# Kernel optimization log

Measured on AMD Instinct MI355X. Metric: run time of the kernel, lower is better.

## Reference

```python
import jax, jax.numpy as jnp
import numpy as np

N_HEADS, HEAD_D, N_LVL, N_PTS, EMB = 8, 32, 1, 4, 256


def _grid_sample(img, grid):
    """Bilinear grid_sample, align_corners=False, zeros padding.
    img: [N,C,H,W], grid: [N,Hg,Wg,2] in [-1,1] (x=width, y=height)."""
    N, C, H, W = img.shape
    x = (grid[..., 0] + 1.0) * (W * 0.5) - 0.5
    y = (grid[..., 1] + 1.0) * (H * 0.5) - 0.5
    x0 = jnp.floor(x); y0 = jnp.floor(y)
    x1 = x0 + 1.0; y1 = y0 + 1.0
    wx1 = x - x0; wx0 = 1.0 - wx1
    wy1 = y - y0; wy0 = 1.0 - wy1
    img_flat = img.reshape(N, C, H * W)

    def gather(xi, yi, w):
        xii = xi.astype(jnp.int32); yii = yi.astype(jnp.int32)
        valid = (xii >= 0) & (xii < W) & (yii >= 0) & (yii < H)
        lin = jnp.clip(yii, 0, H - 1) * W + jnp.clip(xii, 0, W - 1)   # [N,Hg,Wg]
        vals = jnp.take_along_axis(img_flat, lin.reshape(N, 1, -1), axis=2)
        vals = vals.reshape(N, C, lin.shape[1], lin.shape[2])
        return vals * (w * valid)[:, None]

    return (gather(x0, y0, wx0 * wy0) + gather(x1, y0, wx1 * wy0)
            + gather(x0, y1, wx0 * wy1) + gather(x1, y1, wx1 * wy1))


def setup_inputs() -> dict:
    key = jax.random.key(0)
    ks = jax.random.split(key, 16)
    bs, nq, Hl, Wl = 4, 10000, 100, 100
    nv = Hl * Wl
    s = 0.02
    return {
        "query": jax.random.normal(ks[0], (bs, nq, EMB), jnp.float32),
        "key": jax.random.normal(ks[1], (bs, nv, EMB), jnp.float32),
        "value": jax.random.normal(ks[2], (bs, nv, EMB), jnp.float32),
        "reference_points": jax.random.uniform(ks[3], (bs, nq, N_LVL, 2), jnp.float32),
        "Wq": s * jax.random.normal(ks[4], (HEAD_D, HEAD_D), jnp.float32),
        "bq": jnp.zeros((HEAD_D,), jnp.float32),
        "Wk": s * jax.random.normal(ks[5], (HEAD_D, HEAD_D), jnp.float32),
        "bk": jnp.zeros((HEAD_D,), jnp.float32),
        "Wv": s * jax.random.normal(ks[6], (HEAD_D, HEAD_D), jnp.float32),
        "bv": jnp.zeros((HEAD_D,), jnp.float32),
        "Woff": s * jax.random.normal(ks[7], (N_LVL * N_PTS * 2, HEAD_D), jnp.float32),
        "boff": jnp.zeros((N_LVL * N_PTS * 2,), jnp.float32),
        "Wo": s * jax.random.normal(ks[8], (EMB, EMB), jnp.float32),
        "bo": jnp.zeros((EMB,), jnp.float32),
        "spatial_shapes": jnp.array([[Hl, Wl]], dtype=jnp.int32),
    }


def reference(query, key, value, reference_points, Wq, bq, Wk, bk, Wv, bv,
              Woff, boff, Wo, bo, spatial_shapes):
    nH, D, nL, nP = N_HEADS, HEAD_D, N_LVL, N_PTS
    bs, nq, _ = query.shape
    ss = np.asarray(spatial_shapes)                      # static [L,2] (H,W)
    residual = query
    qh = query.reshape(bs, nq, nH, D)
    kh = key.reshape(bs, -1, nH, D)
    vh = value.reshape(bs, -1, nH, D)
    norm = jnp.asarray(np.stack([ss[:, 1], ss[:, 0]], -1), jnp.float32)  # (W,H) per level
    off = (qh @ Woff.T + boff).reshape(bs, nq, nH, nL, nP, 2)
    loc = reference_points[:, :, None, :, None, :] + off / norm[None, None, None, :, None, :]
    grids = 2.0 * loc - 1.0                              # [b,q,h,L,P,2]
    k_parts, v_parts = [], []
    start = 0
    for l in range(nL):
        Hl, Wl = int(ss[l, 0]), int(ss[l, 1])
        sl = slice(start, start + Hl * Wl); start += Hl * Wl
        k_img = kh[:, sl].reshape(bs, Hl * Wl, nH * D).transpose(0, 2, 1).reshape(bs * nH, D, Hl, Wl)
        v_img = vh[:, sl].reshape(bs, Hl * Wl, nH * D).transpose(0, 2, 1).reshape(bs * nH, D, Hl, Wl)
        # NOTE: key grid uses only the FIRST query's sampling locations (as in source: grids[:, :1])
        gk = grids[:, :1, :, l].transpose(0, 2, 1, 3, 4).reshape(bs * nH, 1, nP, 2)
        gv = grids[:, :, :, l].transpose(0, 2, 1, 3, 4).reshape(bs * nH, nq, nP, 2)
        k_parts.append(_grid_sample(k_img, gk))          # [bH, D, 1, P]
        v_parts.append(_grid_sample(v_img, gv))          # [bH, D, nq, P]
    k_samp = jnp.stack(k_parts, axis=-2).reshape(bs * nH, D, nL * nP)
    k_samp = k_samp.reshape(bs, nH, D, nL * nP).transpose(0, 3, 1, 2)     # [b, LP, h, d]
    v_samp = jnp.stack(v_parts, axis=-2).reshape(bs * nH, D, nq, nL * nP)  # [bH, d, q, LP]
    q = qh @ Wq.T + bq                                                    # [b, q, h, d]
    k = k_samp @ Wk.T + bk                                                # [b, LP, h, d]
    v = (v_samp.transpose(0, 2, 3, 1) @ Wv.T + bv).transpose(0, 3, 1, 2)  # [bH, d, q, LP]
    attn = jax.nn.softmax(jnp.einsum('bqhd,bkhd->bqhk', q, k), axis=-1)   # [b, q, h, LP]
    attn = attn.transpose(0, 2, 1, 3).reshape(bs * nH, 1, nq, nL * nP)
    out = (v * attn).sum(-1).reshape(bs, nH * D, nq).transpose(0, 2, 1)   # [b, q, E]
    return out @ Wo.T + bo + residual  # dropout is identity in eval mode
```

## Files before the change

### kernel.cpp

```cpp
#include <hip/hip_runtime.h>
#include <hip/hip_bf16.h>
#include <math.h>

#define NH   8
#define HD   32
#define NP   4
#define EMB  256
#define IMG_H 100
#define IMG_W 100
#define NQ   10000
#define NV   10000
#define BS   4

#define W4S 36
#define TS  2
#define TPL (IMG_W / TS)
#define TPB (TPL * TPL)

#define FENCE() asm volatile("" ::: "memory")

typedef __attribute__((ext_vector_type(8))) short bf16x8;
typedef __attribute__((ext_vector_type(4))) float f32x4;

#define KT_OFF    0
#define KB_OFF    16384
#define BO2_OFF   17408
#define WCF_OFF   18432
#define WCB_OFF   (18432 + 262144)
#define CNT_OFF   (WCB_OFF + 131072)
#define OFF_OFF   (CNT_OFF + 40000)
#define QIDX_OFF  (OFF_OFF + 40000)
#define PREB_OFF  ((QIDX_OFF + 160000 + 63) & ~63ULL)
#define WS_SORT   ((size_t)QIDX_OFF + 160000)
#define WS_FULL   ((size_t)PREB_OFF + (size_t)BS * NQ * EMB * 2)

__global__ __launch_bounds__(64) void k1_keys(
    const float* __restrict__ query, const float* __restrict__ key,
    const float* __restrict__ refp,  const float* __restrict__ Woff,
    const float* __restrict__ boff,  const float* __restrict__ Wk,
    const float* __restrict__ bk,    const float* __restrict__ Wq,
    const float* __restrict__ bq,
    float* __restrict__ kt, float* __restrict__ kb)
{
    int b = blockIdx.x >> 3, h = blockIdx.x & 7;
    __shared__ float q0[HD];
    __shared__ float off[8];
    __shared__ float ks[NP][HD];
    __shared__ float kkl[NP][HD];
    int l = threadIdx.x;

    if (l < HD) q0[l] = query[(size_t)(b * NQ) * EMB + h * HD + l];
    __syncthreads();

    if (l < 8) {
        float s = boff[l];
        #pragma unroll
        for (int d = 0; d < HD; ++d) s += q0[d] * Woff[l * HD + d];
        off[l] = s;
    }
    __syncthreads();

    if (l < HD) {
        float refx = refp[(size_t)(b * NQ) * 2 + 0];
        float refy = refp[(size_t)(b * NQ) * 2 + 1];
        for (int p = 0; p < NP; ++p) {
            float x = refx * IMG_W + off[p * 2 + 0] - 0.5f;
            float y = refy * IMG_H + off[p * 2 + 1] - 0.5f;
            float x0f = floorf(x), y0f = floorf(y);
            int ix0 = (int)x0f, iy0 = (int)y0f;
            float fx = x - x0f, fy = y - y0f;
            float acc = 0.f;
            #pragma unroll
            for (int cy = 0; cy < 2; ++cy)
                #pragma unroll
                for (int cx = 0; cx < 2; ++cx) {
                    int xi = ix0 + cx, yi = iy0 + cy;
                    if ((unsigned)xi < IMG_W && (unsigned)yi < IMG_H) {
                        float wgt = (cx ? fx : 1.f - fx) * (cy ? fy : 1.f - fy);
                        acc += wgt * key[((size_t)b * NV + yi * IMG_W + xi) * EMB + h * HD + l];
                    }
                }
            ks[p][l] = acc;
        }
    }
    __syncthreads();

    #pragma unroll
    for (int t = 0; t < 2; ++t) {
        int idx = l + 64 * t;
        int p = idx >> 5, dout = idx & 31;
        float s = bk[dout];
        #pragma unroll
        for (int d = 0; d < HD; ++d) s += Wk[dout * HD + d] * ks[p][d];
        kkl[p][dout] = s;
    }
    __syncthreads();

    #pragma unroll
    for (int t = 0; t < 2; ++t) {
        int idx = l + 64 * t;
        int p = idx >> 5, d = idx & 31;
        float s = 0.f;
        #pragma unroll
        for (int dd = 0; dd < HD; ++dd) s += Wq[dd * HD + d] * kkl[p][dd];
        kt[((b * NP + p) * NH + h) * HD + d] = s;
    }
    if (l < NP) {
        float s = 0.f;
        #pragma unroll
        for (int dd = 0; dd < HD; ++dd) s += bq[dd] * kkl[l][dd];
        kb[(b * NP + l) * NH + h] = s;
    }
}

__global__ __launch_bounds__(256) void kcomb(
    const float* __restrict__ Wo, const float* __restrict__ Wv,
    const float* __restrict__ bv, const float* __restrict__ bo,
    float* __restrict__ wcf, __hip_bfloat16* __restrict__ wcb,
    float* __restrict__ bo2)
{
    __shared__ float sWv[HD * HD];
    __shared__ float sWoR[EMB];
    __shared__ float sws[4];
    int e = blockIdx.x, col = threadIdx.x;
    *(float4*)&sWv[col * 4] = *(const float4*)(Wv + col * 4);
    sWoR[col] = Wo[(size_t)e * EMB + col];
    __syncthreads();

    int h = col >> 5, d = col & 31;
    float s = 0.f;
    #pragma unroll
    for (int dd = 0; dd < HD; ++dd) s += sWoR[h * HD + dd] * sWv[dd * HD + d];
    wcf[(size_t)e * EMB + col] = s;
    if (wcb) wcb[(size_t)e * EMB + col] = __float2bfloat16(s);

    float pb = bv[d] * sWoR[col];
    #pragma unroll
    for (int o = 1; o < 64; o <<= 1) pb += __shfl_xor(pb, o);
    if ((col & 63) == 0) sws[col >> 6] = pb;
    __syncthreads();
    if (col == 0) bo2[e] = bo[e] + sws[0] + sws[1] + sws[2] + sws[3];
}

__device__ __forceinline__ int tile_of(const float* refp, int gq) {
    float rx = refp[(size_t)gq * 2 + 0];
    float ry = refp[(size_t)gq * 2 + 1];
    int px = min(max((int)(rx * IMG_W), 0), IMG_W - 1);
    int py = min(max((int)(ry * IMG_H), 0), IMG_H - 1);
    return (py / TS) * TPL + (px / TS);
}

__global__ __launch_bounds__(256) void ksort_count(
    const float* __restrict__ refp, int* __restrict__ cnt)
{
    int gq = blockIdx.x * 256 + threadIdx.x;
    if (gq < BS * NQ) {
        int b = gq / NQ;
        atomicAdd(&cnt[b * TPB + tile_of(refp, gq)], 1);
    }
}

__global__ __launch_bounds__(64) void ksort_scan(
    const int* __restrict__ cnt, int* __restrict__ off)
{
    int b = blockIdx.x, lane = threadIdx.x;
    const int PER = (TPB + 63) / 64;
    int lsum[PER];
    int s = 0;
    #pragma unroll
    for (int i = 0; i < PER; ++i) {
        int t = lane * PER + i;
        int c = (t < TPB) ? cnt[b * TPB + t] : 0;
        lsum[i] = s; s += c;
    }
    int inc = s;
    #pragma unroll
    for (int o = 1; o < 64; o <<= 1) {
        int v = __shfl_up(inc, o);
        if (lane >= o) inc += v;
    }
    int excl = inc - s;
    #pragma unroll
    for (int i = 0; i < PER; ++i) {
        int t = lane * PER + i;
        if (t < TPB) off[b * TPB + t] = b * NQ + excl + lsum[i];
    }
}

__global__ __launch_bounds__(256) void ksort_scatter(
    const float* __restrict__ refp, int* __restrict__ off, int* __restrict__ qidx)
{
    int gq = blockIdx.x * 256 + threadIdx.x;
    if (gq < BS * NQ) {
        int b = gq / NQ;
        int slot = atomicAdd(&off[b * TPB + tile_of(refp, gq)], 1);
        qidx[slot] = gq;
    }
}

template<int BF16OUT>
__global__ __launch_bounds__(256) void k2s(
    const float* __restrict__ query, const float* __restrict__ value,
    const float* __restrict__ refp,
    const float* __restrict__ Woff, const float* __restrict__ boff,
    const float* __restrict__ kt, const float* __restrict__ kb,
    const int* __restrict__ qidx,
    float* __restrict__ pre, __hip_bfloat16* __restrict__ preb)
{
    __shared__ float sWoff[8 * W4S];
    __shared__ float sboff[8];
    __shared__ float skt[NP * NH * W4S];
    __shared__ float skb[NP * NH];
    __shared__ float qld[4][NH * W4S];
    __shared__ float offs[4][64];
    __shared__ float attnw[4][32];
    __shared__ int   soff4[4][32][4];
    __shared__ float swgt4[4][32][4];

    int tid = threadIdx.x;

    int bid = blockIdx.x;
    int wg = (bid & 7) * (BS * NQ / 4 / 8) + (bid >> 3);
    int b0 = (wg * 4) / NQ;

    for (int i = tid; i < 8 * HD; i += 256) sWoff[(i >> 5) * W4S + (i & 31)] = Woff[i];
    if (tid < 8)  sboff[tid] = boff[tid];
    {
        int j = tid * 4;
        *(float4*)&skt[(j >> 5) * W4S + (j & 31)] =
            *(const float4*)(kt + b0 * (NP * NH * HD) + j);
    }
    if (tid < NP * NH) skb[tid] = kb[b0 * (NP * NH) + tid];

    int w = tid >> 6, lane = tid & 63;
    int gq = qidx ? qidx[wg * 4 + w] : (wg * 4 + w);
    int b = b0;

    float4 qv = *(const float4*)(query + (size_t)gq * EMB + lane * 4);
    { int e = lane * 4; *(float4*)&qld[w][(e >> 5) * W4S + (e & 31)] = qv; }
    float refx = refp[(size_t)gq * 2 + 0];
    float refy = refp[(size_t)gq * 2 + 1];
    __syncthreads();

    int h = lane >> 3, t = lane & 7;

    float qr[HD];
    #pragma unroll
    for (int d = 0; d < HD; d += 4) {
        float4 v4 = *(const float4*)&qld[w][h * W4S + d];
        qr[d] = v4.x; qr[d + 1] = v4.y; qr[d + 2] = v4.z; qr[d + 3] = v4.w;
    }

    {
        float s = sboff[t];
        const float* wr = &sWoff[t * W4S];
        #pragma unroll
        for (int d = 0; d < HD; d += 4) {
            float4 ww = *(const float4*)(wr + d);
            s += qr[d]*ww.x + qr[d+1]*ww.y + qr[d+2]*ww.z + qr[d+3]*ww.w;
        }
        offs[w][h * 8 + t] = s;
    }

    float plog[NP];
    #pragma unroll
    for (int p = 0; p < NP; ++p) {
        const float* kr = &skt[(p * NH + h) * W4S];
        float s = 0.f;
        #pragma unroll
        for (int k = 0; k < 4; ++k) s += qr[t + 8 * k] * kr[t + 8 * k];
        plog[p] = s;
    }
    #pragma unroll
    for (int p = 0; p < NP; ++p) {
        plog[p] += __shfl_xor(plog[p], 1, 8);
        plog[p] += __shfl_xor(plog[p], 2, 8);
        plog[p] += __shfl_xor(plog[p], 4, 8);
        plog[p] += skb[p * NH + h];
    }
    {
        float mm = fmaxf(fmaxf(plog[0], plog[1]), fmaxf(plog[2], plog[3]));
        float e0 = __expf(plog[0]-mm), e1 = __expf(plog[1]-mm);
        float e2 = __expf(plog[2]-mm), e3 = __expf(plog[3]-mm);
        float inv = 1.f / (e0 + e1 + e2 + e3);
        if (t < 4) {
            float a = (t == 0) ? e0 : (t == 1) ? e1 : (t == 2) ? e2 : e3;
            attnw[w][h * 4 + t] = a * inv;
        }
    }
    FENCE();

    if (lane < 32) {
        int h2 = lane >> 2, p = lane & 3;
        float x = refx * IMG_W + offs[w][h2 * 8 + p * 2 + 0] - 0.5f;
        float y = refy * IMG_H + offs[w][h2 * 8 + p * 2 + 1] - 0.5f;
        float x0f = floorf(x), y0f = floorf(y);
        int ix0 = (int)x0f, iy0 = (int)y0f;
        float fx = x - x0f, fy = y - y0f;
        float aw = attnw[w][lane];
        float wx1 = fx * aw, wx0 = aw - wx1;
        int bbase = b * (NV * EMB) + h2 * HD;
        int   o4[4]; float g4[4];
        #pragma unroll
        for (int c = 0; c < 4; ++c) {
            int cx = c & 1, cy = c >> 1;
            int xi = ix0 + cx, yi = iy0 + cy;
            bool valid = ((unsigned)xi < IMG_W) & ((unsigned)yi < IMG_H);
            int xc = min(max(xi, 0), IMG_W - 1);
            int yc = min(max(yi, 0), IMG_H - 1);
            o4[c] = (bbase + (yc * IMG_W + xc) * EMB) * 4;
            float wv = (cx ? wx1 : wx0) * (cy ? fy : 1.f - fy);
            g4[c] = valid ? wv : 0.f;
        }
        int4   ov = {o4[0], o4[1], o4[2], o4[3]};
        float4 gv = {g4[0], g4[1], g4[2], g4[3]};
        *(int4*)&soff4[w][lane][0]   = ov;
        *(float4*)&swgt4[w][lane][0] = gv;
    }
    FENCE();

    {
        unsigned co = t * 16;
        const char* vb = (const char*)value;
        float4 acc = {0.f, 0.f, 0.f, 0.f};
        #pragma unroll
        for (int p = 0; p < NP; ++p) {
            int hp = h * 4 + p;
            int4   o4 = *(const int4*)&soff4[w][hp][0];
            float4 g4 = *(const float4*)&swgt4[w][hp][0];
            float4 v0 = *(const float4*)(vb + (unsigned)o4.x + co);
            float4 v1 = *(const float4*)(vb + (unsigned)o4.y + co);
            float4 v2 = *(const float4*)(vb + (unsigned)o4.z + co);
            float4 v3 = *(const float4*)(vb + (unsigned)o4.w + co);
            acc.x += g4.x*v0.x + g4.y*v1.x + g4.z*v2.x + g4.w*v3.x;
            acc.y += g4.x*v0.y + g4.y*v1.y + g4.z*v2.y + g4.w*v3.y;
            acc.z += g4.x*v0.z + g4.y*v1.z + g4.z*v2.z + g4.w*v3.z;
            acc.w += g4.x*v0.w + g4.y*v1.w + g4.z*v2.w + g4.w*v3.w;
        }
        int cb = t * 4;
        if (BF16OUT) {
            __hip_bfloat16 pk[4];
            pk[0] = __float2bfloat16(acc.x);
            pk[1] = __float2bfloat16(acc.y);
            pk[2] = __float2bfloat16(acc.z);
            pk[3] = __float2bfloat16(acc.w);
            *(ushort4*)((unsigned short*)preb + (size_t)gq * EMB + h * HD + cb) =
                *(const ushort4*)&pk[0];
        } else {
            *(float4*)(pre + (size_t)gq * EMB + h * HD + cb) = acc;
        }
    }
}

__global__ __launch_bounds__(256) void k3_mfma(
    const __hip_bfloat16* __restrict__ preb, const __hip_bfloat16* __restrict__ wcb,
    float* __restrict__ outp, const float* __restrict__ query,
    const float* __restrict__ bo2)
{
    int w = threadIdx.x >> 6, lane = threadIdx.x & 63;
    size_t m0 = (size_t)blockIdx.x * 64;
    int n0 = w * 64;
    int lr = lane & 15, lg = lane >> 4;

    const short* pa = (const short*)preb;
    const short* pb = (const short*)wcb;

    f32x4 acc[4][4];
    #pragma unroll
    for (int mt = 0; mt < 4; ++mt)
        #pragma unroll
        for (int nt = 0; nt < 4; ++nt) acc[mt][nt] = (f32x4){0.f, 0.f, 0.f, 0.f};

    #pragma unroll
    for (int k0 = 0; k0 < EMB; k0 += 32) {
        bf16x8 af[4], bf[4];
        #pragma unroll
        for (int mt = 0; mt < 4; ++mt)
            af[mt] = *(const bf16x8*)(pa + (m0 + mt * 16 + lr) * EMB + k0 + lg * 8);
        #pragma unroll
        for (int nt = 0; nt < 4; ++nt)
            bf[nt] = *(const bf16x8*)(pb + (size_t)(n0 + nt * 16 + lr) * EMB + k0 + lg * 8);
        #pragma unroll
        for (int mt = 0; mt < 4; ++mt)
            #pragma unroll
            for (int nt = 0; nt < 4; ++nt)
                acc[mt][nt] = __builtin_amdgcn_mfma_f32_16x16x32_bf16(
                    af[mt], bf[nt], acc[mt][nt], 0, 0, 0);
    }

    float bov[4];
    #pragma unroll
    for (int nt = 0; nt < 4; ++nt) bov[nt] = bo2[n0 + nt * 16 + lr];

    #pragma unroll
    for (int mt = 0; mt < 4; ++mt)
        #pragma unroll
        for (int q = 0; q < 4; ++q) {
            size_t row = m0 + mt * 16 + lg * 4 + q;
            const float* qrow = query + row * EMB;
            float* orow = outp + row * EMB;
            #pragma unroll
            for (int nt = 0; nt < 4; ++nt) {
                int col = n0 + nt * 16 + lr;
                orow[col] = acc[mt][nt][q] + bov[nt] + qrow[col];
            }
        }
}

__global__ __launch_bounds__(256) void k3_gemm(
    const float* __restrict__ pre, float* __restrict__ outp,
    const float* __restrict__ query, const float* __restrict__ wcf,
    const float* __restrict__ bo2)
{
    __shared__ float As[64 * EMB];
    int tid = threadIdx.x;
    size_t r0 = (size_t)blockIdx.x * 64;
    {
        const float4* src = (const float4*)(pre + r0 * EMB);
        float4* dst = (float4*)As;
        for (int i = tid; i < 64 * EMB / 4; i += 256) dst[i] = src[i];
    }
    __syncthreads();

    int w = tid >> 6, lane = tid & 63;
    int rb = w * 16;
    float acc[16][4];
    #pragma unroll
    for (int r = 0; r < 16; ++r)
        #pragma unroll
        for (int j = 0; j < 4; ++j) acc[r][j] = 0.f;

    for (int kc = 0; kc < EMB / 4; ++kc) {
        float4 wreg[4];
        #pragma unroll
        for (int j = 0; j < 4; ++j)
            wreg[j] = *(const float4*)&wcf[(size_t)(lane + 64 * j) * EMB + kc * 4];
        #pragma unroll
        for (int r = 0; r < 16; ++r) {
            float4 a = *(const float4*)&As[(rb + r) * EMB + kc * 4];
            #pragma unroll
            for (int j = 0; j < 4; ++j)
                acc[r][j] += a.x * wreg[j].x + a.y * wreg[j].y
                           + a.z * wreg[j].z + a.w * wreg[j].w;
        }
    }

    #pragma unroll
    for (int r = 0; r < 16; ++r) {
        size_t row = r0 + rb + r;
        #pragma unroll
        for (int j = 0; j < 4; ++j) {
            int c = lane + 64 * j;
            outp[row * EMB + c] = acc[r][j] + bo2[c] + query[row * EMB + c];
        }
    }
}

extern "C" void kernel_launch(void* const* d_in, const int* in_sizes, int n_in,
                              void* d_out, int out_size, void* d_ws, size_t ws_size,
                              hipStream_t stream) {
    const float* query = (const float*)d_in[0];
    const float* key   = (const float*)d_in[1];
    const float* value = (const float*)d_in[2];
    const float* refp  = (const float*)d_in[3];
    const float* Wq   = (const float*)d_in[4];
    const float* bq   = (const float*)d_in[5];
    const float* Wk   = (const float*)d_in[6];
    const float* bk   = (const float*)d_in[7];
    const float* Wv   = (const float*)d_in[8];
    const float* bv   = (const float*)d_in[9];
    const float* Woff = (const float*)d_in[10];
    const float* boff = (const float*)d_in[11];
    const float* Wo   = (const float*)d_in[12];
    const float* bo   = (const float*)d_in[13];
    (void)in_sizes; (void)n_in; (void)out_size;

    float* out = (float*)d_out;
    char*  ws  = (char*)d_ws;
    float* kt  = (float*)(ws + KT_OFF);
    float* kb  = (float*)(ws + KB_OFF);
    float* bo2 = (float*)(ws + BO2_OFF);
    float* wcf = (float*)(ws + WCF_OFF);
    __hip_bfloat16* wcb = (__hip_bfloat16*)(ws + WCB_OFF);

    bool have_sort = (ws_size >= WS_SORT);
    int* cnt  = (int*)(ws + CNT_OFF);
    int* off  = (int*)(ws + OFF_OFF);
    int* qidx = have_sort ? (int*)(ws + QIDX_OFF) : nullptr;

    if (have_sort) hipMemsetAsync(cnt, 0, BS * TPB * sizeof(int), stream);

    k1_keys<<<BS * NH, 64, 0, stream>>>(query, key, refp, Woff, boff, Wk, bk,
                                        Wq, bq, kt, kb);
    kcomb<<<EMB, 256, 0, stream>>>(Wo, Wv, bv, bo, wcf, wcb, bo2);

    if (have_sort) {
        int nthr = (BS * NQ + 255) / 256;
        ksort_count<<<nthr, 256, 0, stream>>>(refp, cnt);
        ksort_scan<<<BS, 64, 0, stream>>>(cnt, off);
        ksort_scatter<<<nthr, 256, 0, stream>>>(refp, off, qidx);
    }

    if (ws_size >= WS_FULL) {
        __hip_bfloat16* preb = (__hip_bfloat16*)(ws + PREB_OFF);
        k2s<1><<<BS * NQ / 4, 256, 0, stream>>>(query, value, refp, Woff, boff,
                                                kt, kb, qidx, nullptr, preb);
        k3_mfma<<<BS * NQ / 64, 256, 0, stream>>>(preb, wcb, out, query, bo2);
    } else {
        k2s<0><<<BS * NQ / 4, 256, 0, stream>>>(query, value, refp, Woff, boff,
                                                kt, kb, qidx, out, nullptr);
        k3_gemm<<<BS * NQ / 64, 256, 0, stream>>>(out, out, query, wcf, bo2);
    }
}
```

Measured before the change: 101.2 us.

## Process queries per spatial tile with an LDS-staged value window

Replaces the per-query sampling kernel with one block per 2x2 reference tile. Each block stages a 4x4 pixel window of the value tensor into LDS and loops over the queries sorted into that tile. Bilinear samples that fall inside the window read from LDS, and any wave with an out-of-window sample falls back to global loads. Separately, the key-prep and weight-combine kernels are merged into one launch to cut launch overhead. The risks are uneven per-tile query counts, a larger LDS footprint that lowers occupancy, and blocks that exit early on empty tiles.

```diff
diff --git a/kernel.cpp b/kernel.cpp
--- a/kernel.cpp
+++ b/kernel.cpp
@@ -16,6 +16,7 @@
 #define TS  2
 #define TPL (IMG_W / TS)
 #define TPB (TPL * TPL)
+#define HS  520
 
 #define FENCE() asm volatile("" ::: "memory")
 
@@ -31,115 +32,110 @@
 #define OFF_OFF   (CNT_OFF + 40000)
 #define QIDX_OFF  (OFF_OFF + 40000)
 #define PREB_OFF  ((QIDX_OFF + 160000 + 63) & ~63ULL)
-#define WS_SORT   ((size_t)QIDX_OFF + 160000)
 #define WS_FULL   ((size_t)PREB_OFF + (size_t)BS * NQ * EMB * 2)
 
-__global__ __launch_bounds__(64) void k1_keys(
+__global__ __launch_bounds__(256) void kprep(
     const float* __restrict__ query, const float* __restrict__ key,
     const float* __restrict__ refp,  const float* __restrict__ Woff,
     const float* __restrict__ boff,  const float* __restrict__ Wk,
     const float* __restrict__ bk,    const float* __restrict__ Wq,
     const float* __restrict__ bq,
-    float* __restrict__ kt, float* __restrict__ kb)
-{
-    int b = blockIdx.x >> 3, h = blockIdx.x & 7;
-    __shared__ float q0[HD];
-    __shared__ float off[8];
-    __shared__ float ks[NP][HD];
-    __shared__ float kkl[NP][HD];
-    int l = threadIdx.x;
-
-    if (l < HD) q0[l] = query[(size_t)(b * NQ) * EMB + h * HD + l];
-    __syncthreads();
-
-    if (l < 8) {
-        float s = boff[l];
-        #pragma unroll
-        for (int d = 0; d < HD; ++d) s += q0[d] * Woff[l * HD + d];
-        off[l] = s;
-    }
-    __syncthreads();
-
-    if (l < HD) {
-        float refx = refp[(size_t)(b * NQ) * 2 + 0];
-        float refy = refp[(size_t)(b * NQ) * 2 + 1];
-        for (int p = 0; p < NP; ++p) {
-            float x = refx * IMG_W + off[p * 2 + 0] - 0.5f;
-            float y = refy * IMG_H + off[p * 2 + 1] - 0.5f;
-            float x0f = floorf(x), y0f = floorf(y);
-            int ix0 = (int)x0f, iy0 = (int)y0f;
-            float fx = x - x0f, fy = y - y0f;
-            float acc = 0.f;
-            #pragma unroll
-            for (int cy = 0; cy < 2; ++cy)
-                #pragma unroll
-                for (int cx = 0; cx < 2; ++cx) {
-                    int xi = ix0 + cx, yi = iy0 + cy;
-                    if ((unsigned)xi < IMG_W && (unsigned)yi < IMG_H) {
-                        float wgt = (cx ? fx : 1.f - fx) * (cy ? fy : 1.f - fy);
-                        acc += wgt * key[((size_t)b * NV + yi * IMG_W + xi) * EMB + h * HD + l];
-                    }
-                }
-            ks[p][l] = acc;
-        }
-    }
-    __syncthreads();
-
-    #pragma unroll
-    for (int t = 0; t < 2; ++t) {
-        int idx = l + 64 * t;
-        int p = idx >> 5, dout = idx & 31;
-        float s = bk[dout];
-        #pragma unroll
-        for (int d = 0; d < HD; ++d) s += Wk[dout * HD + d] * ks[p][d];
-        kkl[p][dout] = s;
-    }
-    __syncthreads();
-
-    #pragma unroll
-    for (int t = 0; t < 2; ++t) {
-        int idx = l + 64 * t;
-        int p = idx >> 5, d = idx & 31;
-        float s = 0.f;
-        #pragma unroll
-        for (int dd = 0; dd < HD; ++dd) s += Wq[dd * HD + d] * kkl[p][dd];
-        kt[((b * NP + p) * NH + h) * HD + d] = s;
-    }
-    if (l < NP) {
-        float s = 0.f;
-        #pragma unroll
-        for (int dd = 0; dd < HD; ++dd) s += bq[dd] * kkl[l][dd];
-        kb[(b * NP + l) * NH + h] = s;
-    }
-}
-
-__global__ __launch_bounds__(256) void kcomb(
     const float* __restrict__ Wo, const float* __restrict__ Wv,
     const float* __restrict__ bv, const float* __restrict__ bo,
+    float* __restrict__ kt, float* __restrict__ kb,
     float* __restrict__ wcf, __hip_bfloat16* __restrict__ wcb,
     float* __restrict__ bo2)
 {
-    __shared__ float sWv[HD * HD];
-    __shared__ float sWoR[EMB];
-    __shared__ float sws[4];
-    int e = blockIdx.x, col = threadIdx.x;
-    *(float4*)&sWv[col * 4] = *(const float4*)(Wv + col * 4);
-    sWoR[col] = Wo[(size_t)e * EMB + col];
-    __syncthreads();
-
-    int h = col >> 5, d = col & 31;
-    float s = 0.f;
-    #pragma unroll
-    for (int dd = 0; dd < HD; ++dd) s += sWoR[h * HD + dd] * sWv[dd * HD + d];
-    wcf[(size_t)e * EMB + col] = s;
-    if (wcb) wcb[(size_t)e * EMB + col] = __float2bfloat16(s);
-
-    float pb = bv[d] * sWoR[col];
-    #pragma unroll
-    for (int o = 1; o < 64; o <<= 1) pb += __shfl_xor(pb, o);
-    if ((col & 63) == 0) sws[col >> 6] = pb;
-    __syncthreads();
-    if (col == 0) bo2[e] = bo[e] + sws[0] + sws[1] + sws[2] + sws[3];
+    if (blockIdx.x < EMB) {
+        __shared__ float sWv[HD * HD];
+        __shared__ float sWoR[EMB];
+        __shared__ float sws[4];
+        int e = blockIdx.x, col = threadIdx.x;
+        *(float4*)&sWv[col * 4] = *(const float4*)(Wv + col * 4);
+        sWoR[col] = Wo[(size_t)e * EMB + col];
+        __syncthreads();
+
+        int d = col & 31;
+        float s = 0.f;
+        #pragma unroll
+        for (int dd = 0; dd < HD; ++dd) s += sWoR[(col >> 5) * HD + dd] * sWv[dd * HD + d];
+        wcf[(size_t)e * EMB + col] = s;
+        if (wcb) wcb[(size_t)e * EMB + col] = __float2bfloat16(s);
+
+        float pb = bv[d] * sWoR[col];
+        #pragma unroll
+        for (int o = 1; o < 64; o <<= 1) pb += __shfl_xor(pb, o);
+        if ((col & 63) == 0) sws[col >> 6] = pb;
+        __syncthreads();
+        if (col == 0) bo2[e] = bo[e] + sws[0] + sws[1] + sws[2] + sws[3];
+    } else {
+        int bh = blockIdx.x - EMB;
+        int b = bh >> 3, h = bh & 7;
+        __shared__ float q0[HD];
+        __shared__ float off[8];
+        __shared__ float ks[NP][HD];
+        __shared__ float kkl[NP][HD];
+        int l = threadIdx.x;
+
+        if (l < HD) q0[l] = query[(size_t)(b * NQ) * EMB + h * HD + l];
+        __syncthreads();
+
+        if (l < 8) {
+            float s = boff[l];
+            #pragma unroll
+            for (int d = 0; d < HD; ++d) s += q0[d] * Woff[l * HD + d];
+            off[l] = s;
+        }
+        __syncthreads();
+
+        if (l < HD) {
+            float refx = refp[(size_t)(b * NQ) * 2 + 0];
+            float refy = refp[(size_t)(b * NQ) * 2 + 1];
+            for (int p = 0; p < NP; ++p) {
+                float x = refx * IMG_W + off[p * 2 + 0] - 0.5f;
+                float y = refy * IMG_H + off[p * 2 + 1] - 0.5f;
+                float x0f = floorf(x), y0f = floorf(y);
+                int ix0 = (int)x0f, iy0 = (int)y0f;
+                float fx = x - x0f, fy = y - y0f;
+                float acc = 0.f;
+                #pragma unroll
+                for (int cy = 0; cy < 2; ++cy)
+                    #pragma unroll
+                    for (int cx = 0; cx < 2; ++cx) {
+                        int xi = ix0 + cx, yi = iy0 + cy;
+                        if ((unsigned)xi < IMG_W && (unsigned)yi < IMG_H) {
+                            float wgt = (cx ? fx : 1.f - fx) * (cy ? fy : 1.f - fy);
+                            acc += wgt * key[((size_t)b * NV + yi * IMG_W + xi) * EMB + h * HD + l];
+                        }
+                    }
+                ks[p][l] = acc;
+            }
+        }
+        __syncthreads();
+
+        if (l < 128) {
+            int p = l >> 5, dout = l & 31;
+            float s = bk[dout];
+            #pragma unroll
+            for (int d = 0; d < HD; ++d) s += Wk[dout * HD + d] * ks[p][d];
+            kkl[p][dout] = s;
+        }
+        __syncthreads();
+
+        if (l < 128) {
+            int p = l >> 5, d = l & 31;
+            float s = 0.f;
+            #pragma unroll
+            for (int dd = 0; dd < HD; ++dd) s += Wq[dd * HD + d] * kkl[p][dd];
+            kt[((b * NP + p) * NH + h) * HD + d] = s;
+        }
+        if (l < NP) {
+            float s = 0.f;
+            #pragma unroll
+            for (int dd = 0; dd < HD; ++dd) s += bq[dd] * kkl[l][dd];
+            kb[(b * NP + l) * NH + h] = s;
+        }
+    }
 }
 
 __device__ __forceinline__ int tile_of(const float* refp, int gq) {
@@ -161,7 +157,7 @@
 }
 
 __global__ __launch_bounds__(64) void ksort_scan(
-    const int* __restrict__ cnt, int* __restrict__ off)
+    const int* __restrict__ cnt, int* __restrict__ offarr)
 {
     int b = blockIdx.x, lane = threadIdx.x;
     const int PER = (TPB + 63) / 64;
@@ -183,29 +179,228 @@
     #pragma unroll
     for (int i = 0; i < PER; ++i) {
         int t = lane * PER + i;
-        if (t < TPB) off[b * TPB + t] = b * NQ + excl + lsum[i];
+        if (t < TPB) offarr[b * TPB + t] = b * NQ + excl + lsum[i];
     }
 }
 
 __global__ __launch_bounds__(256) void ksort_scatter(
-    const float* __restrict__ refp, int* __restrict__ off, int* __restrict__ qidx)
+    const float* __restrict__ refp, int* __restrict__ offarr, int* __restrict__ qidx)
 {
     int gq = blockIdx.x * 256 + threadIdx.x;
     if (gq < BS * NQ) {
         int b = gq / NQ;
-        int slot = atomicAdd(&off[b * TPB + tile_of(refp, gq)], 1);
+        int slot = atomicAdd(&offarr[b * TPB + tile_of(refp, gq)], 1);
         qidx[slot] = gq;
     }
 }
 
-template<int BF16OUT>
+__global__ __launch_bounds__(256) void k2t(
+    const float* __restrict__ query, const float* __restrict__ value,
+    const float* __restrict__ refp,
+    const float* __restrict__ Woff, const float* __restrict__ boff,
+    const float* __restrict__ kt, const float* __restrict__ kb,
+    const int* __restrict__ cnt, const int* __restrict__ offarr,
+    const int* __restrict__ qidx, __hip_bfloat16* __restrict__ preb)
+{
+    __shared__ float winL[8 * HS];
+    __shared__ float sWoff[8 * W4S];
+    __shared__ int   soff4[4][32][4];
+    __shared__ float swgt4[4][32][4];
+
+    int tid = threadIdx.x;
+
+    int bid = blockIdx.x;
+    int wg = (bid & 7) * (BS * TPB / 8) + (bid >> 3);
+    int b = wg / TPB;
+    int tile = wg - b * TPB;
+    int tx = tile % TPL, ty = tile / TPL;
+    int x0i = tx * TS - 1, y0i = ty * TS - 1;
+
+    int n = cnt[b * TPB + tile];
+    if (n == 0) return;
+    int cend = offarr[b * TPB + tile];
+    int qstart = cend - n;
+
+    int w = tid >> 6, lane = tid & 63;
+    int h = lane >> 3, t = lane & 7;
+
+    for (int i = tid; i < 8 * HD; i += 256) sWoff[(i >> 5) * W4S + (i & 31)] = Woff[i];
+    float boffr = boff[t];
+
+    float ktr[16];
+    #pragma unroll
+    for (int p = 0; p < NP; ++p)
+        #pragma unroll
+        for (int k = 0; k < 4; ++k)
+            ktr[p * 4 + k] = kt[((b * NP + p) * NH + h) * HD + t + 8 * k];
+    float kbr[4];
+    #pragma unroll
+    for (int p = 0; p < NP; ++p) kbr[p] = kb[(b * NP + p) * NH + h];
+
+    {
+        int px = tid >> 4, m = tid & 15;
+        int wx = px & 3, wy = px >> 2;
+        int xc = min(max(x0i + wx, 0), IMG_W - 1);
+        int yc = min(max(y0i + wy, 0), IMG_H - 1);
+        const float* src = value + ((size_t)(b * NV) + yc * IMG_W + xc) * EMB + m * 16;
+        int c0 = m * 16;
+        int dst = (c0 >> 5) * HS + px * 32 + (c0 & 31);
+        #pragma unroll
+        for (int i = 0; i < 4; ++i) {
+            float4 v = *(const float4*)(src + i * 4);
+            *(float4*)&winL[dst + i * 4] = v;
+        }
+    }
+    __syncthreads();
+
+    for (int qi = qstart + w; qi < cend; qi += 4) {
+        int gq = qidx[qi];
+
+        float qr[HD];
+        const float* qrow = query + (size_t)gq * EMB + h * HD;
+        #pragma unroll
+        for (int d = 0; d < HD; d += 4) {
+            float4 v4 = *(const float4*)(qrow + d);
+            qr[d] = v4.x; qr[d + 1] = v4.y; qr[d + 2] = v4.z; qr[d + 3] = v4.w;
+        }
+        float refx = refp[(size_t)gq * 2 + 0];
+        float refy = refp[(size_t)gq * 2 + 1];
+
+        float offv = boffr;
+        {
+            const float* wr = &sWoff[t * W4S];
+            #pragma unroll
+            for (int d = 0; d < HD; d += 4) {
+                float4 ww = *(const float4*)(wr + d);
+                offv += qr[d]*ww.x + qr[d+1]*ww.y + qr[d+2]*ww.z + qr[d+3]*ww.w;
+            }
+        }
+
+        float plog[NP];
+        #pragma unroll
+        for (int p = 0; p < NP; ++p) {
+            float s = 0.f;
+            #pragma unroll
+            for (int k = 0; k < 4; ++k) s += qr[t + 8 * k] * ktr[p * 4 + k];
+            plog[p] = s;
+        }
+        #pragma unroll
+        for (int p = 0; p < NP; ++p) {
+            plog[p] += __shfl_xor(plog[p], 1, 8);
+            plog[p] += __shfl_xor(plog[p], 2, 8);
+            plog[p] += __shfl_xor(plog[p], 4, 8);
+            plog[p] += kbr[p];
+        }
+        float aval = 0.f;
+        {
+            float mm = fmaxf(fmaxf(plog[0], plog[1]), fmaxf(plog[2], plog[3]));
+            float e0 = __expf(plog[0]-mm), e1 = __expf(plog[1]-mm);
+            float e2 = __expf(plog[2]-mm), e3 = __expf(plog[3]-mm);
+            float inv = 1.f / (e0 + e1 + e2 + e3);
+            if (t < 4) aval = ((t == 0) ? e0 : (t == 1) ? e1 : (t == 2) ? e2 : e3) * inv;
+        }
+
+        int h2 = (lane & 31) >> 2, p2 = lane & 3;
+        float mox = __shfl(offv, h2 * 8 + 2 * p2);
+        float moy = __shfl(offv, h2 * 8 + 2 * p2 + 1);
+        float maw = __shfl(aval, h2 * 8 + p2);
+        bool inwin = true;
+        if (lane < 32) {
+            float x = refx * IMG_W + mox - 0.5f;
+            float y = refy * IMG_H + moy - 0.5f;
+            float x0f = floorf(x), y0f = floorf(y);
+            int ix0 = (int)x0f, iy0 = (int)y0f;
+            int wx0 = ix0 - x0i, wy0 = iy0 - y0i;
+            inwin = ((unsigned)wx0 <= 2u) & ((unsigned)wy0 <= 2u);
+            if (inwin) {
+                float fx = x - x0f, fy = y - y0f;
+                float wx1 = fx * maw, wxz = maw - wx1;
+                int   o4[4]; float g4[4];
+                #pragma unroll
+                for (int c = 0; c < 4; ++c) {
+                    int cx = c & 1, cy = c >> 1;
+                    int xi = ix0 + cx, yi = iy0 + cy;
+                    bool valid = ((unsigned)xi < IMG_W) & ((unsigned)yi < IMG_H);
+                    int px = (wy0 + cy) * 4 + (wx0 + cx);
+                    o4[c] = px * 32;
+                    float wv = (cx ? wx1 : wxz) * (cy ? fy : 1.f - fy);
+                    g4[c] = valid ? wv : 0.f;
+                }
+                int4   ov = {o4[0], o4[1], o4[2], o4[3]};
+                float4 gv = {g4[0], g4[1], g4[2], g4[3]};
+                *(int4*)&soff4[w][lane][0]   = ov;
+                *(float4*)&swgt4[w][lane][0] = gv;
+            }
+        }
+        unsigned long long obal = __ballot(!inwin);
+        FENCE();
+
+        float4 acc = {0.f, 0.f, 0.f, 0.f};
+        if (obal == 0ULL) {
+            int base = h * HS + t * 4;
+            #pragma unroll
+            for (int p = 0; p < NP; ++p) {
+                int hp = h * 4 + p;
+                int4   o4 = *(const int4*)&soff4[w][hp][0];
+                float4 g4 = *(const float4*)&swgt4[w][hp][0];
+                float4 v0 = *(const float4*)&winL[base + o4.x];
+                float4 v1 = *(const float4*)&winL[base + o4.y];
+                float4 v2 = *(const float4*)&winL[base + o4.z];
+                float4 v3 = *(const float4*)&winL[base + o4.w];
+                acc.x += g4.x*v0.x + g4.y*v1.x + g4.z*v2.x + g4.w*v3.x;
+                acc.y += g4.x*v0.y + g4.y*v1.y + g4.z*v2.y + g4.w*v3.y;
+                acc.z += g4.x*v0.z + g4.y*v1.z + g4.z*v2.z + g4.w*v3.z;
+                acc.w += g4.x*v0.w + g4.y*v1.w + g4.z*v2.w + g4.w*v3.w;
+            }
+        } else {
+            #pragma unroll
+            for (int p = 0; p < NP; ++p) {
+                float ox = __shfl(offv, h * 8 + 2 * p);
+                float oy = __shfl(offv, h * 8 + 2 * p + 1);
+                float aw = __shfl(aval, h * 8 + p);
+                float x = refx * IMG_W + ox - 0.5f;
+                float y = refy * IMG_H + oy - 0.5f;
+                float x0f = floorf(x), y0f = floorf(y);
+                int ix0 = (int)x0f, iy0 = (int)y0f;
+                float fx = x - x0f, fy = y - y0f;
+                float wx1 = fx * aw, wxz = aw - wx1;
+                #pragma unroll
+                for (int c = 0; c < 4; ++c) {
+                    int cx = c & 1, cy = c >> 1;
+                    int xi = ix0 + cx, yi = iy0 + cy;
+                    bool valid = ((unsigned)xi < IMG_W) & ((unsigned)yi < IMG_H);
+                    int xc = min(max(xi, 0), IMG_W - 1);
+                    int yc = min(max(yi, 0), IMG_H - 1);
+                    float g = (cx ? wx1 : wxz) * (cy ? fy : 1.f - fy);
+                    g = valid ? g : 0.f;
+                    const float* vsrc = value + ((size_t)(b * NV) + yc * IMG_W + xc) * EMB
+                                      + h * HD + t * 4;
+                    float4 v = *(const float4*)vsrc;
+                    acc.x += g * v.x; acc.y += g * v.y;
+                    acc.z += g * v.z; acc.w += g * v.w;
+                }
+            }
+        }
+
+        {
+            __hip_bfloat16 pk[4];
+            pk[0] = __float2bfloat16(acc.x);
+            pk[1] = __float2bfloat16(acc.y);
+            pk[2] = __float2bfloat16(acc.z);
+            pk[3] = __float2bfloat16(acc.w);
+            *(ushort4*)((unsigned short*)preb + (size_t)gq * EMB + h * HD + t * 4) =
+                *(const ushort4*)&pk[0];
+        }
+        FENCE();
+    }
+}
+
 __global__ __launch_bounds__(256) void k2s(
     const float* __restrict__ query, const float* __restrict__ value,
     const float* __restrict__ refp,
     const float* __restrict__ Woff, const float* __restrict__ boff,
     const float* __restrict__ kt, const float* __restrict__ kb,
-    const int* __restrict__ qidx,
-    float* __restrict__ pre, __hip_bfloat16* __restrict__ preb)
+    float* __restrict__ pre)
 {
     __shared__ float sWoff[8 * W4S];
     __shared__ float sboff[8];
@@ -218,10 +413,7 @@
     __shared__ float swgt4[4][32][4];
 
     int tid = threadIdx.x;
-
-    int bid = blockIdx.x;
-    int wg = (bid & 7) * (BS * NQ / 4 / 8) + (bid >> 3);
-    int b0 = (wg * 4) / NQ;
+    int b0 = (blockIdx.x * 4) / NQ;
 
     for (int i = tid; i < 8 * HD; i += 256) sWoff[(i >> 5) * W4S + (i & 31)] = Woff[i];
     if (tid < 8)  sboff[tid] = boff[tid];
@@ -233,7 +425,7 @@
     if (tid < NP * NH) skb[tid] = kb[b0 * (NP * NH) + tid];
 
     int w = tid >> 6, lane = tid & 63;
-    int gq = qidx ? qidx[wg * 4 + w] : (wg * 4 + w);
+    int gq = blockIdx.x * 4 + w;
     int b = b0;
 
     float4 qv = *(const float4*)(query + (size_t)gq * EMB + lane * 4);
@@ -250,7 +442,6 @@
         float4 v4 = *(const float4*)&qld[w][h * W4S + d];
         qr[d] = v4.x; qr[d + 1] = v4.y; qr[d + 2] = v4.z; qr[d + 3] = v4.w;
     }
-
     {
         float s = sboff[t];
         const float* wr = &sWoff[t * W4S];
@@ -261,7 +452,6 @@
         }
         offs[w][h * 8 + t] = s;
     }
-
     float plog[NP];
     #pragma unroll
     for (int p = 0; p < NP; ++p) {
@@ -289,7 +479,6 @@
         }
     }
     FENCE();
-
     if (lane < 32) {
         int h2 = lane >> 2, p = lane & 3;
         float x = refx * IMG_W + offs[w][h2 * 8 + p * 2 + 0] - 0.5f;
@@ -318,7 +507,6 @@
         *(float4*)&swgt4[w][lane][0] = gv;
     }
     FENCE();
-
     {
         unsigned co = t * 16;
         const char* vb = (const char*)value;
@@ -337,18 +525,7 @@
             acc.z += g4.x*v0.z + g4.y*v1.z + g4.z*v2.z + g4.w*v3.z;
             acc.w += g4.x*v0.w + g4.y*v1.w + g4.z*v2.w + g4.w*v3.w;
         }
-        int cb = t * 4;
-        if (BF16OUT) {
-            __hip_bfloat16 pk[4];
-            pk[0] = __float2bfloat16(acc.x);
-            pk[1] = __float2bfloat16(acc.y);
-            pk[2] = __float2bfloat16(acc.z);
-            pk[3] = __float2bfloat16(acc.w);
-            *(ushort4*)((unsigned short*)preb + (size_t)gq * EMB + h * HD + cb) =
-                *(const ushort4*)&pk[0];
-        } else {
-            *(float4*)(pre + (size_t)gq * EMB + h * HD + cb) = acc;
-        }
+        *(float4*)(pre + (size_t)gq * EMB + h * HD + t * 4) = acc;
     }
 }
 
@@ -483,32 +660,32 @@
     float* wcf = (float*)(ws + WCF_OFF);
     __hip_bfloat16* wcb = (__hip_bfloat16*)(ws + WCB_OFF);
 
-    bool have_sort = (ws_size >= WS_SORT);
-    int* cnt  = (int*)(ws + CNT_OFF);
-    int* off  = (int*)(ws + OFF_OFF);
-    int* qidx = have_sort ? (int*)(ws + QIDX_OFF) : nullptr;
-
-    if (have_sort) hipMemsetAsync(cnt, 0, BS * TPB * sizeof(int), stream);
-
-    k1_keys<<<BS * NH, 64, 0, stream>>>(query, key, refp, Woff, boff, Wk, bk,
-                                        Wq, bq, kt, kb);
-    kcomb<<<EMB, 256, 0, stream>>>(Wo, Wv, bv, bo, wcf, wcb, bo2);
-
-    if (have_sort) {
+    bool full = (ws_size >= WS_FULL);
+
+    if (full) {
+        int* cnt  = (int*)(ws + CNT_OFF);
+        int* offa = (int*)(ws + OFF_OFF);
+        int* qidx = (int*)(ws + QIDX_OFF);
+        __hip_bfloat16* preb = (__hip_bfloat16*)(ws + PREB_OFF);
+
+        hipMemsetAsync(cnt, 0, BS * TPB * sizeof(int), stream);
+        kprep<<<EMB + BS * NH, 256, 0, stream>>>(query, key, refp, Woff, boff, Wk, bk,
+                                                 Wq, bq, Wo, Wv, bv, bo,
+                                                 kt, kb, wcf, wcb, bo2);
         int nthr = (BS * NQ + 255) / 256;
         ksort_count<<<nthr, 256, 0, stream>>>(refp, cnt);
-        ksort_scan<<<BS, 64, 0, stream>>>(cnt, off);
-        ksort_scatter<<<nthr, 256, 0, stream>>>(refp, off, qidx);
-    }
-
-    if (ws_size >= WS_FULL) {
-        __hip_bfloat16* preb = (__hip_bfloat16*)(ws + PREB_OFF);
-        k2s<1><<<BS * NQ / 4, 256, 0, stream>>>(query, value, refp, Woff, boff,
-                                                kt, kb, qidx, nullptr, preb);
+        ksort_scan<<<BS, 64, 0, stream>>>(cnt, offa);
+        ksort_scatter<<<nthr, 256, 0, stream>>>(refp, offa, qidx);
+
+        k2t<<<BS * TPB, 256, 0, stream>>>(query, value, refp, Woff, boff,
+                                          kt, kb, cnt, offa, qidx, preb);
         k3_mfma<<<BS * NQ / 64, 256, 0, stream>>>(preb, wcb, out, query, bo2);
     } else {
-        k2s<0><<<BS * NQ / 4, 256, 0, stream>>>(query, value, refp, Woff, boff,
-                                                kt, kb, qidx, out, nullptr);
+        kprep<<<EMB + BS * NH, 256, 0, stream>>>(query, key, refp, Woff, boff, Wk, bk,
+                                                 Wq, bq, Wo, Wv, bv, bo,
+                                                 kt, kb, wcf, nullptr, bo2);
+        k2s<<<BS * NQ / 4, 256, 0, stream>>>(query, value, refp, Woff, boff,
+                                             kt, kb, out);
         k3_gemm<<<BS * NQ / 64, 256, 0, stream>>>(out, out, query, wcf, bo2);
     }
 }
```

After: 145.2 us. 43.6% more time.
